# Kernel optimization log

Measured on AMD Instinct MI355X. Metric: run time of the kernel, lower is better.

## Reference

```python
import jax, jax.numpy as jnp
import numpy as np

N, F_IN, D_MID, D_HID, H, G, D_TGT = 6144, 128, 128, 64, 4, 12, 16
LEAKY_ALPHA = 0.2
EPS = 1e-9


def setup_inputs() -> dict:
    key = jax.random.key(0)
    ks = jax.random.split(key, 12)
    x = jax.random.normal(ks[0], (N, F_IN), dtype=jnp.float32)
    # 12 graphs of 512 nodes each (sorted segment ids)
    batch = jnp.repeat(jnp.arange(G, dtype=jnp.int32), N // G)
    # counting_attn is block-diagonal per graph with nonnegative random walk counts
    block = (batch[:, None] == batch[None, :]).astype(jnp.float32)
    counting_attn = jax.random.uniform(ks[1], (N, N), dtype=jnp.float32) * block
    s = lambda d: 1.0 / np.sqrt(d).astype(np.float32)
    Wv = jax.random.normal(ks[2], (F_IN, D_MID), jnp.float32) * s(F_IN)
    bv = jnp.zeros((D_MID,), jnp.float32)
    W0 = jax.random.normal(ks[3], (H, D_MID, D_HID), jnp.float32) * s(D_MID)
    al0 = jax.random.normal(ks[4], (H, D_HID), jnp.float32) * s(D_HID)
    ar0 = jax.random.normal(ks[5], (H, D_HID), jnp.float32) * s(D_HID)
    Wf = jax.random.normal(ks[6], (H * D_HID, D_MID), jnp.float32) * s(H * D_HID)
    alf = jax.random.normal(ks[7], (D_MID,), jnp.float32) * s(D_MID)
    arf = jax.random.normal(ks[8], (D_MID,), jnp.float32) * s(D_MID)
    W1 = jax.random.normal(ks[9], (D_MID, D_MID), jnp.float32) * s(D_MID)
    b1 = jnp.zeros((D_MID,), jnp.float32)
    W2 = jax.random.normal(ks[10], (D_MID, D_TGT), jnp.float32) * s(D_MID)
    b2 = jnp.zeros((D_TGT,), jnp.float32)
    return dict(x=x, counting_attn=counting_attn, batch=batch,
                Wv=Wv, bv=bv, W0=W0, al0=al0, ar0=ar0,
                Wf=Wf, alf=alf, arf=arf, W1=W1, b1=b1, W2=W2, b2=b2)


def gwk_head(h, mask, W, al, ar):
    # GWKLayer: elementwise score, LeakyReLU, masked softmax (via max-sub + exp*mask), weighted sum, ELU
    ft = h @ W  # [N, D]
    a1 = jnp.einsum('nd,d->n', ft, al)  # [N]
    a2 = jnp.einsum('nd,d->n', ft, ar)  # [N]
    a = jax.nn.leaky_relu(a1[:, None] + a2[None, :], LEAKY_ALPHA)  # [N, N]
    a = a - jnp.max(a, axis=1, keepdims=True)
    nomi = jnp.exp(a) * mask
    attn = nomi / (jnp.sum(nomi, axis=1, keepdims=True) + EPS)
    return jax.nn.elu(attn @ ft)  # [N, D]


def reference(x, counting_attn, batch, Wv, bv, W0, al0, ar0, Wf, alf, arf, W1, b1, W2, b2):
    # normalize == 'ones' -> no-op; dropout p = 0.0 (eval)
    h = jax.nn.relu(x @ Wv + bv)  # fc_before_gat: [N, D_MID]
    # layer 0: H parallel heads, concatenated along feature dim
    heads = jax.vmap(lambda W, al, ar: gwk_head(h, counting_attn, W, al, ar))(W0, al0, ar0)  # [H, N, D_HID]
    h = jnp.transpose(heads, (1, 0, 2)).reshape(N, H * D_HID)  # [N, 256]
    # final single-head layer back to D_MID
    h = gwk_head(h, counting_attn, Wf, alf, arf)  # [N, D_MID]
    # pooling 'mean' dispatches to global_add_pool (sum per graph) in the source
    pooled = jax.ops.segment_sum(h, batch, num_segments=G)  # [G, D_MID]
    out = jax.nn.relu(pooled @ W1 + b1) @ W2 + b2  # [G, D_TGT]
    return out
```

## Files before the change

### kernel.cpp

```cpp
#include <hip/hip_runtime.h>
#include <math.h>

#define Nn 6144
#define FIN 128
#define DMID 128
#define DHID 64
#define NH 4
#define NG 12
#define NB 512
#define ALPHA 0.2f
#define EPSV 1e-9f

typedef __bf16 bf16x8 __attribute__((ext_vector_type(8)));
typedef float f32x4 __attribute__((ext_vector_type(4)));
typedef unsigned short ushort_t;

union BU { bf16x8 v; uint u[4]; uint4 q; };

__device__ __forceinline__ float leaky(float x){ return x > 0.f ? x : ALPHA*x; }
__device__ __forceinline__ float eluf(float x){ return x > 0.f ? x : __expf(x)-1.f; }
__device__ __forceinline__ uint f2bf(float f){
  uint u = __float_as_uint(f);
  return (u + 0x7FFFu + ((u>>16)&1u)) >> 16;
}
__device__ __forceinline__ float wave_max(float v){
  #pragma unroll
  for (int off=32; off; off>>=1) v = fmaxf(v, __shfl_xor(v, off));
  return v;
}

__global__ __launch_bounds__(256) void k_prep(
    const float* __restrict__ Wv, const float* __restrict__ W0, const float* __restrict__ Wf,
    ushort_t* __restrict__ WvS, ushort_t* __restrict__ W0S, ushort_t* __restrict__ WfS){
  int tid = blockIdx.x*256 + threadIdx.x;
  int lane = tid & 63, blk = tid >> 6;
  if (blk >= 160) return;
  const float* src; ushort_t* dst; int N; size_t off;
  if (blk < 32){
    int nt = blk>>2, kt = blk&3;
    src = Wv; dst = WvS; N = 128;
    off = ((size_t)(nt*4+kt)*64 + lane)*8;
    int col = nt*16 + (lane&15); int k0 = kt*32 + (lane>>4)*8;
    uint4 pk;
    uint e0=f2bf(src[(k0+0)*N+col]), e1=f2bf(src[(k0+1)*N+col]);
    uint e2=f2bf(src[(k0+2)*N+col]), e3=f2bf(src[(k0+3)*N+col]);
    uint e4=f2bf(src[(k0+4)*N+col]), e5=f2bf(src[(k0+5)*N+col]);
    uint e6=f2bf(src[(k0+6)*N+col]), e7=f2bf(src[(k0+7)*N+col]);
    pk.x=e0|(e1<<16); pk.y=e2|(e3<<16); pk.z=e4|(e5<<16); pk.w=e6|(e7<<16);
    *reinterpret_cast<uint4*>(dst + off) = pk;
  } else if (blk < 96){
    int b2 = blk-32; int hd = b2>>4, r = b2&15; int nt = r>>2, kt = r&3;
    src = W0 + (size_t)hd*128*64; dst = W0S + (size_t)hd*8192; N = 64;
    off = ((size_t)(nt*4+kt)*64 + lane)*8;
    int col = nt*16 + (lane&15); int k0 = kt*32 + (lane>>4)*8;
    uint4 pk;
    uint e0=f2bf(src[(k0+0)*N+col]), e1=f2bf(src[(k0+1)*N+col]);
    uint e2=f2bf(src[(k0+2)*N+col]), e3=f2bf(src[(k0+3)*N+col]);
    uint e4=f2bf(src[(k0+4)*N+col]), e5=f2bf(src[(k0+5)*N+col]);
    uint e6=f2bf(src[(k0+6)*N+col]), e7=f2bf(src[(k0+7)*N+col]);
    pk.x=e0|(e1<<16); pk.y=e2|(e3<<16); pk.z=e4|(e5<<16); pk.w=e6|(e7<<16);
    *reinterpret_cast<uint4*>(dst + off) = pk;
  } else {
    int b2 = blk-96; int nt = b2>>3, kt = b2&7;
    src = Wf; dst = WfS; N = 128;
    off = ((size_t)(nt*8+kt)*64 + lane)*8;
    int col = nt*16 + (lane&15); int k0 = kt*32 + (lane>>4)*8;
    uint4 pk;
    uint e0=f2bf(src[(k0+0)*N+col]), e1=f2bf(src[(k0+1)*N+col]);
    uint e2=f2bf(src[(k0+2)*N+col]), e3=f2bf(src[(k0+3)*N+col]);
    uint e4=f2bf(src[(k0+4)*N+col]), e5=f2bf(src[(k0+5)*N+col]);
    uint e6=f2bf(src[(k0+6)*N+col]), e7=f2bf(src[(k0+7)*N+col]);
    pk.x=e0|(e1<<16); pk.y=e2|(e3<<16); pk.z=e4|(e5<<16); pk.w=e6|(e7<<16);
    *reinterpret_cast<uint4*>(dst + off) = pk;
  }
}

__global__ __launch_bounds__(256) void k_f1(
    const float* __restrict__ x, const float* __restrict__ bv,
    const ushort_t* __restrict__ WvS, const ushort_t* __restrict__ W0S,
    const float* __restrict__ al0, const float* __restrict__ ar0,
    ushort_t* __restrict__ ftS, float* __restrict__ a1arr, float* __restrict__ a2arr,
    float* __restrict__ pmax0){
  int b = blockIdx.x; int i0 = b*16;
  int t = threadIdx.x, lane = t&63, w = t>>6;
  int row = lane&15, kg = lane>>4;
  __shared__ ushort_t xs[16][136];
  __shared__ ushort_t hts[16][136];
  __shared__ ushort_t fts[16][264];
  {
    const float* xp = x + (size_t)i0*FIN + t*8;
    float4 f0 = *reinterpret_cast<const float4*>(xp);
    float4 f1 = *reinterpret_cast<const float4*>(xp+4);
    uint4 pk;
    pk.x = f2bf(f0.x)|(f2bf(f0.y)<<16); pk.y = f2bf(f0.z)|(f2bf(f0.w)<<16);
    pk.z = f2bf(f1.x)|(f2bf(f1.y)<<16); pk.w = f2bf(f1.z)|(f2bf(f1.w)<<16);
    *reinterpret_cast<uint4*>(&xs[t>>4][(t&15)*8]) = pk;
  }
  __syncthreads();
  {
    f32x4 acc2[2] = {{0,0,0,0},{0,0,0,0}};
    #pragma unroll
    for (int kt=0; kt<4; ++kt){
      bf16x8 aF = *reinterpret_cast<bf16x8*>(&xs[row][kt*32 + kg*8]);
      #pragma unroll
      for (int e2=0; e2<2; ++e2){
        int nt = w*2+e2;
        BU B; B.q = *reinterpret_cast<const uint4*>(WvS + ((size_t)(nt*4+kt)*64 + lane)*8);
        acc2[e2] = __builtin_amdgcn_mfma_f32_16x16x32_bf16(aF, B.v, acc2[e2], 0, 0, 0);
      }
    }
    #pragma unroll
    for (int e2=0; e2<2; ++e2){
      int nt = w*2+e2;
      float bvv = bv[nt*16+row];
      #pragma unroll
      for (int reg=0; reg<4; ++reg){
        float v = fmaxf(acc2[e2][reg]+bvv, 0.f);
        hts[kg*4+reg][nt*16+row] = (ushort_t)f2bf(v);
      }
    }
  }
  __syncthreads();
  f32x4 acc4[4] = {{0,0,0,0},{0,0,0,0},{0,0,0,0},{0,0,0,0}};
  #pragma unroll
  for (int kt=0; kt<4; ++kt){
    bf16x8 aF = *reinterpret_cast<bf16x8*>(&hts[row][kt*32 + kg*8]);
    #pragma unroll
    for (int nt=0; nt<4; ++nt){
      BU B; B.q = *reinterpret_cast<const uint4*>(W0S + ((size_t)((w*4+nt)*4+kt)*64 + lane)*8);
      acc4[nt] = __builtin_amdgcn_mfma_f32_16x16x32_bf16(aF, B.v, acc4[nt], 0, 0, 0);
    }
  }
  {
    float alv[4], arv[4];
    #pragma unroll
    for (int nt=0; nt<4; ++nt){ alv[nt] = al0[w*DHID+nt*16+row]; arv[nt] = ar0[w*DHID+nt*16+row]; }
    float s1[4]={0,0,0,0}, s2[4]={0,0,0,0};
    #pragma unroll
    for (int nt=0; nt<4; ++nt)
      #pragma unroll
      for (int reg=0; reg<4; ++reg){
        s1[reg] += acc4[nt][reg]*alv[nt];
        s2[reg] += acc4[nt][reg]*arv[nt];
      }
    #pragma unroll
    for (int off=1; off<16; off<<=1)
      #pragma unroll
      for (int reg=0; reg<4; ++reg){
        s1[reg] += __shfl_xor(s1[reg], off);
        s2[reg] += __shfl_xor(s2[reg], off);
      }
    if (row==0){
      #pragma unroll
      for (int reg=0; reg<4; ++reg){
        a1arr[w*Nn + i0 + kg*4+reg] = s1[reg];
        a2arr[w*Nn + i0 + kg*4+reg] = s2[reg];
      }
    }
    float mm = fmaxf(fmaxf(s2[0],s2[1]), fmaxf(s2[2],s2[3]));
    mm = fmaxf(mm, __shfl_xor(mm,16));
    mm = fmaxf(mm, __shfl_xor(mm,32));
    if (lane==0) pmax0[w*384 + b] = mm;
  }
  #pragma unroll
  for (int nt=0; nt<4; ++nt)
    #pragma unroll
    for (int reg=0; reg<4; ++reg)
      fts[kg*4+reg][w*DHID + nt*16+row] = (ushort_t)f2bf(acc4[nt][reg]);
  __syncthreads();
  {
    int ch = t, hd2 = ch>>6, ct = (ch>>4)&3, c = ch&15;
    int g = b>>5, ktj = (b&31)>>1, half = b&1;
    ushort_t v[16];
    #pragma unroll
    for (int i=0; i<16; ++i) v[i] = fts[i][ch];
    uint4 p0, p1;
    p0.x=(uint)v[0]|((uint)v[1]<<16);  p0.y=(uint)v[2]|((uint)v[3]<<16);
    p0.z=(uint)v[4]|((uint)v[5]<<16);  p0.w=(uint)v[6]|((uint)v[7]<<16);
    p1.x=(uint)v[8]|((uint)v[9]<<16);  p1.y=(uint)v[10]|((uint)v[11]<<16);
    p1.z=(uint)v[12]|((uint)v[13]<<16);p1.w=(uint)v[14]|((uint)v[15]<<16);
    size_t base = (((size_t)(g*4+hd2)*16 + ktj)*4 + ct)*512;
    *reinterpret_cast<uint4*>(ftS + base + ((half*2+0)*16+c)*8) = p0;
    *reinterpret_cast<uint4*>(ftS + base + ((half*2+1)*16+c)*8) = p1;
  }
}

__global__ __launch_bounds__(512) void k_attn0fcf(
    const ushort_t* __restrict__ ftS, const float* __restrict__ a1arr,
    const float* __restrict__ a2arr, const float* __restrict__ pmax0,
    const float* __restrict__ mask, const ushort_t* __restrict__ WfS,
    const float* __restrict__ alf, const float* __restrict__ arf,
    ushort_t* __restrict__ ftfS, float* __restrict__ a1f, float* __restrict__ a2f,
    float* __restrict__ pmaxf){
  int b = blockIdx.x;
  int g = b>>5, it = b&31;
  int i0 = g*NB + it*16, jbase = g*NB;
  int t = threadIdx.x, lane = t&63, w = t>>6;
  int hd = w>>1, jh = w&1;
  int row = lane&15, kg = lane>>4;

  __shared__ float aacc[8][4][64][4];
  __shared__ float ad[8][16];
  __shared__ ushort_t h1s[16][264];
  __shared__ ushort_t fts[16][136];
  __shared__ float dpA[8][16], dpB[8][16];

  {
    float mxv = -INFINITY;
    #pragma unroll
    for (int q=0; q<6; ++q) mxv = fmaxf(mxv, pmax0[hd*384 + q*64 + lane]);
    mxv = wave_max(mxv);
    float a1v = a1arr[hd*Nn + i0 + row];
    float mv = leaky(a1v + mxv);
    f32x4 acc[4] = {{0,0,0,0},{0,0,0,0},{0,0,0,0},{0,0,0,0}};
    float dsum = 0.f;
    const float* mrow = mask + (size_t)(i0+row)*Nn;
    size_t fbase = ((size_t)(g*4+hd)*16*4)*512;
    #pragma unroll 2
    for (int c8=0; c8<8; ++c8){
      int kt = jh*8 + c8;
      int jc = jbase + kt*32 + kg*8;
      float4 mk0 = *reinterpret_cast<const float4*>(mrow + jc);
      float4 mk1 = *reinterpret_cast<const float4*>(mrow + jc + 4);
      float4 a20 = *reinterpret_cast<const float4*>(a2arr + hd*Nn + jc);
      float4 a21 = *reinterpret_cast<const float4*>(a2arr + hd*Nn + jc + 4);
      float a2l[8] = {a20.x,a20.y,a20.z,a20.w,a21.x,a21.y,a21.z,a21.w};
      float mkl[8] = {mk0.x,mk0.y,mk0.z,mk0.w,mk1.x,mk1.y,mk1.z,mk1.w};
      float wv[8];
      #pragma unroll
      for (int e=0;e<8;++e){
        float p = __expf(leaky(a1v + a2l[e]) - mv) * mkl[e];
        wv[e] = p; dsum += p;
      }
      BU A;
      #pragma unroll
      for (int q=0;q<4;++q) A.u[q] = f2bf(wv[2*q]) | (f2bf(wv[2*q+1])<<16);
      #pragma unroll
      for (int ct=0; ct<4; ++ct){
        BU B; B.q = *reinterpret_cast<const uint4*>(ftS + fbase + (size_t)(kt*4+ct)*512 + lane*8);
        acc[ct] = __builtin_amdgcn_mfma_f32_16x16x32_bf16(A.v, B.v, acc[ct], 0, 0, 0);
      }
    }
    dsum += __shfl_xor(dsum, 16);
    dsum += __shfl_xor(dsum, 32);
    if (lane < 16) ad[w][lane] = dsum;
    #pragma unroll
    for (int ct=0; ct<4; ++ct)
      *reinterpret_cast<float4*>(&aacc[w][ct][lane][0]) = (float4){acc[ct][0],acc[ct][1],acc[ct][2],acc[ct][3]};
  }
  __syncthreads();
  {
    int w0 = hd*2, w1 = hd*2+1;
    float dr[4];
    #pragma unroll
    for (int reg=0; reg<4; ++reg) dr[reg] = ad[w0][kg*4+reg] + ad[w1][kg*4+reg] + EPSV;
    #pragma unroll
    for (int ci=0; ci<2; ++ci){
      int ct = jh*2+ci;
      float4 A0 = *reinterpret_cast<float4*>(&aacc[w0][ct][lane][0]);
      float4 A1 = *reinterpret_cast<float4*>(&aacc[w1][ct][lane][0]);
      float tot[4] = {A0.x+A1.x, A0.y+A1.y, A0.z+A1.z, A0.w+A1.w};
      #pragma unroll
      for (int reg=0; reg<4; ++reg){
        float o = eluf(tot[reg]/dr[reg]);
        h1s[kg*4+reg][hd*64 + ct*16 + row] = (ushort_t)f2bf(o);
      }
    }
  }
  __syncthreads();
  {
    f32x4 acc2 = {0,0,0,0};
    #pragma unroll
    for (int kt=0; kt<8; ++kt){
      bf16x8 aF = *reinterpret_cast<bf16x8*>(&h1s[row][kt*32 + kg*8]);
      BU B; B.q = *reinterpret_cast<const uint4*>(WfS + ((size_t)(w*8+kt)*64 + lane)*8);
      acc2 = __builtin_amdgcn_mfma_f32_16x16x32_bf16(aF, B.v, acc2, 0, 0, 0);
    }
    float alv = alf[w*16+row], arv = arf[w*16+row];
    float s1[4], s2[4];
    #pragma unroll
    for (int reg=0; reg<4; ++reg){
      s1[reg] = acc2[reg]*alv;
      s2[reg] = acc2[reg]*arv;
      fts[kg*4+reg][w*16+row] = (ushort_t)f2bf(acc2[reg]);
    }
    #pragma unroll
    for (int off=1; off<16; off<<=1)
      #pragma unroll
      for (int reg=0; reg<4; ++reg){
        s1[reg] += __shfl_xor(s1[reg], off);
        s2[reg] += __shfl_xor(s2[reg], off);
      }
    if (row==0){
      #pragma unroll
      for (int reg=0; reg<4; ++reg){ dpA[w][kg*4+reg]=s1[reg]; dpB[w][kg*4+reg]=s2[reg]; }
    }
  }
  __syncthreads();
  if (t < 16){
    float v1=0.f, v2=0.f;
    #pragma unroll
    for (int q=0; q<8; ++q){ v1 += dpA[q][t]; v2 += dpB[q][t]; }
    a1f[i0+t] = v1; a2f[i0+t] = v2;
    float m = v2;
    #pragma unroll
    for (int off=1; off<16; off<<=1) m = fmaxf(m, __shfl_xor(m, off));
    if (t==0) pmaxf[b] = m;
  }
  if (t < 256){
    int ch = t>>1, half8 = t&1;
    int ct = ch>>4, c = ch&15;
    int gg = b>>5, ktj = (b&31)>>1, half = b&1;
    ushort_t v[8];
    #pragma unroll
    for (int i=0; i<8; ++i) v[i] = fts[half8*8+i][ch];
    uint4 pk;
    pk.x=(uint)v[0]|((uint)v[1]<<16); pk.y=(uint)v[2]|((uint)v[3]<<16);
    pk.z=(uint)v[4]|((uint)v[5]<<16); pk.w=(uint)v[6]|((uint)v[7]<<16);
    int kslot = half*2 + half8;
    size_t base = ((size_t)(gg*16+ktj)*8 + ct)*512;
    *reinterpret_cast<uint4*>(ftfS + base + (kslot*16+c)*8) = pk;
  }
}

__global__ __launch_bounds__(256) void k_attnf(
    const ushort_t* __restrict__ ftfS, const float* __restrict__ a1f,
    const float* __restrict__ a2f, const float* __restrict__ pmaxf,
    const float* __restrict__ mask, float* __restrict__ ppart){
  int b = blockIdx.x;
  int g = b>>5, it = b&31;
  int i0 = g*NB + it*16, jbase = g*NB;
  int t = threadIdx.x, lane = t&63, w = t>>6;
  int row = lane&15, kg = lane>>4;
  __shared__ float s_acc[4][8][64][4];
  __shared__ float s_d[4][16];
  float mxv = -INFINITY;
  #pragma unroll
  for (int q=0; q<6; ++q) mxv = fmaxf(mxv, pmaxf[q*64 + lane]);
  mxv = wave_max(mxv);
  float a1v = a1f[i0+row];
  float mv = leaky(a1v + mxv);
  f32x4 acc[8];
  #pragma unroll
  for (int ct=0; ct<8; ++ct) acc[ct] = (f32x4){0,0,0,0};
  float dsum = 0.f;
  const float* mrow = mask + (size_t)(i0+row)*Nn;
  #pragma unroll 2
  for (int c4=0; c4<4; ++c4){
    int kt = w*4 + c4;
    int jc = jbase + kt*32 + kg*8;
    float4 mk0 = *reinterpret_cast<const float4*>(mrow + jc);
    float4 mk1 = *reinterpret_cast<const float4*>(mrow + jc + 4);
    float4 a20 = *reinterpret_cast<const float4*>(a2f + jc);
    float4 a21 = *reinterpret_cast<const float4*>(a2f + jc + 4);
    float a2l[8] = {a20.x,a20.y,a20.z,a20.w,a21.x,a21.y,a21.z,a21.w};
    float mkl[8] = {mk0.x,mk0.y,mk0.z,mk0.w,mk1.x,mk1.y,mk1.z,mk1.w};
    float wv[8];
    #pragma unroll
    for (int e=0;e<8;++e){
      float p = __expf(leaky(a1v + a2l[e]) - mv) * mkl[e];
      wv[e] = p; dsum += p;
    }
    BU A;
    #pragma unroll
    for (int q=0;q<4;++q) A.u[q] = f2bf(wv[2*q]) | (f2bf(wv[2*q+1])<<16);
    #pragma unroll
    for (int ct=0; ct<8; ++ct){
      BU B; B.q = *reinterpret_cast<const uint4*>(ftfS + ((size_t)(g*16+kt)*8 + ct)*512 + lane*8);
      acc[ct] = __builtin_amdgcn_mfma_f32_16x16x32_bf16(A.v, B.v, acc[ct], 0, 0, 0);
    }
  }
  dsum += __shfl_xor(dsum, 16);
  dsum += __shfl_xor(dsum, 32);
  if (lane < 16) s_d[w][lane] = dsum;
  #pragma unroll
  for (int ct=0; ct<8; ++ct)
    *reinterpret_cast<float4*>(&s_acc[w][ct][lane][0]) = (float4){acc[ct][0],acc[ct][1],acc[ct][2],acc[ct][3]};
  __syncthreads();
  float dr[4];
  #pragma unroll
  for (int reg=0; reg<4; ++reg)
    dr[reg] = s_d[0][kg*4+reg] + s_d[1][kg*4+reg] + s_d[2][kg*4+reg] + s_d[3][kg*4+reg] + EPSV;
  #pragma unroll
  for (int ci=0; ci<2; ++ci){
    int ct = w*2 + ci;
    float4 A0 = *reinterpret_cast<float4*>(&s_acc[0][ct][lane][0]);
    float4 A1 = *reinterpret_cast<float4*>(&s_acc[1][ct][lane][0]);
    float4 A2 = *reinterpret_cast<float4*>(&s_acc[2][ct][lane][0]);
    float4 A3 = *reinterpret_cast<float4*>(&s_acc[3][ct][lane][0]);
    float tot[4] = {A0.x+A1.x+A2.x+A3.x, A0.y+A1.y+A2.y+A3.y,
                    A0.z+A1.z+A2.z+A3.z, A0.w+A1.w+A2.w+A3.w};
    float psum = 0.f;
    #pragma unroll
    for (int reg=0; reg<4; ++reg) psum += eluf(tot[reg]/dr[reg]);
    psum += __shfl_xor(psum, 16);
    psum += __shfl_xor(psum, 32);
    if (lane < 16) ppart[(size_t)b*DMID + ct*16 + lane] = psum;
  }
}

__global__ __launch_bounds__(256) void k_mlp(
    const float* __restrict__ ppart, const float* __restrict__ W1, const float* __restrict__ b1,
    const float* __restrict__ W2, const float* __restrict__ b2, float* __restrict__ out){
  int g = blockIdx.x;
  int t = threadIdx.x;
  __shared__ float red[8][DMID];
  __shared__ float ps[DMID], ts[DMID];
  __shared__ float p2[2][DMID];
  __shared__ float p4[2][16];
  {
    float4 s4 = {0,0,0,0};
    #pragma unroll
    for (int gi=0; gi<4; ++gi){
      int itx = (t>>5) + gi*8;
      float4 v = *reinterpret_cast<const float4*>(ppart + (size_t)(g*32+itx)*DMID + (t&31)*4);
      s4.x += v.x; s4.y += v.y; s4.z += v.z; s4.w += v.w;
    }
    *reinterpret_cast<float4*>(&red[t>>5][(t&31)*4]) = s4;
  }
  __syncthreads();
  if (t < DMID){
    float s = 0.f;
    #pragma unroll
    for (int q=0; q<8; ++q) s += red[q][t];
    ps[t] = s;
  }
  __syncthreads();
  {
    int col = t & 127, half = t>>7;
    float acc = 0.f;
    #pragma unroll 8
    for (int k=half*64; k<half*64+64; ++k) acc += ps[k]*W1[k*DMID+col];
    p2[half][col] = acc;
  }
  __syncthreads();
  if (t < DMID) ts[t] = fmaxf(p2[0][t]+p2[1][t]+b1[t], 0.f);
  __syncthreads();
  if (t < 32){
    int col = t & 15, half = t>>4;
    float acc = 0.f;
    #pragma unroll 8
    for (int k=half*64; k<half*64+64; ++k) acc += ts[k]*W2[k*16+col];
    p4[half][col] = acc;
  }
  __syncthreads();
  if (t < 16) out[g*16+t] = p4[0][t]+p4[1][t]+b2[t];
}

extern "C" void kernel_launch(void* const* d_in, const int* in_sizes, int n_in,
                              void* d_out, int out_size, void* d_ws, size_t ws_size,
                              hipStream_t stream) {
  const float* x    = (const float*)d_in[0];
  const float* mask = (const float*)d_in[1];
  const float* Wv   = (const float*)d_in[3];
  const float* bv   = (const float*)d_in[4];
  const float* W0   = (const float*)d_in[5];
  const float* al0  = (const float*)d_in[6];
  const float* ar0  = (const float*)d_in[7];
  const float* Wf   = (const float*)d_in[8];
  const float* alf  = (const float*)d_in[9];
  const float* arf  = (const float*)d_in[10];
  const float* W1   = (const float*)d_in[11];
  const float* b1   = (const float*)d_in[12];
  const float* W2   = (const float*)d_in[13];
  const float* b2   = (const float*)d_in[14];
  float* out = (float*)d_out;

  char* W = (char*)d_ws;
  ushort_t* WvS  = (ushort_t*)(W);
  ushort_t* W0S  = (ushort_t*)(W + 32768);
  ushort_t* WfS  = (ushort_t*)(W + 98304);
  ushort_t* ftS  = (ushort_t*)(W + 163840);
  ushort_t* ftfS = (ushort_t*)(W + 3309568);
  float* a1arr = (float*)(W + 4882432);
  float* a2arr = (float*)(W + 4980736);
  float* a1f   = (float*)(W + 5079040);
  float* a2f   = (float*)(W + 5103616);
  float* pmax0 = (float*)(W + 5128192);
  float* pmaxf = (float*)(W + 5134336);
  float* ppart = (float*)(W + 5135872);

  hipLaunchKernelGGL(k_prep,     dim3(40),    dim3(256), 0, stream, Wv, W0, Wf, WvS, W0S, WfS);
  hipLaunchKernelGGL(k_f1,       dim3(Nn/16), dim3(256), 0, stream,
                     x, bv, WvS, W0S, al0, ar0, ftS, a1arr, a2arr, pmax0);
  hipLaunchKernelGGL(k_attn0fcf, dim3(NG*32), dim3(512), 0, stream,
                     ftS, a1arr, a2arr, pmax0, mask, WfS, alf, arf, ftfS, a1f, a2f, pmaxf);
  hipLaunchKernelGGL(k_attnf,    dim3(NG*32), dim3(256), 0, stream,
                     ftfS, a1f, a2f, pmaxf, mask, ppart);
  hipLaunchKernelGGL(k_mlp,      dim3(NG),    dim3(256), 0, stream,
                     ppart, W1, b1, W2, b2, out);
}
```

Baseline: 57.50 us.

## Fuse weight prep into f1 and MLP into final attention via tickets

Removes the separate weight-packing kernel by having each f1 block pack Wv/W0 into shared memory (and 8 blocks pack Wf to global). It also folds the MLP into the last attention kernel, using a per-graph atomic ticket so the last-finishing block does the pooling and MLP. Block count is halved to 192 with 512 threads handling 32 rows each, and the split-j reduction in attn0 is replaced by full-K loops per wave. The aim is fewer launches and less smem reduction traffic. The cost is redundant weight packing in every f1 block and lower grid parallelism.

```diff
diff --git a/kernel.cpp b/kernel.cpp
--- a/kernel.cpp
+++ b/kernel.cpp
@@ -28,113 +28,103 @@
   for (int off=32; off; off>>=1) v = fmaxf(v, __shfl_xor(v, off));
   return v;
 }
-
-__global__ __launch_bounds__(256) void k_prep(
-    const float* __restrict__ Wv, const float* __restrict__ W0, const float* __restrict__ Wf,
-    ushort_t* __restrict__ WvS, ushort_t* __restrict__ W0S, ushort_t* __restrict__ WfS){
-  int tid = blockIdx.x*256 + threadIdx.x;
-  int lane = tid & 63, blk = tid >> 6;
-  if (blk >= 160) return;
-  const float* src; ushort_t* dst; int N; size_t off;
-  if (blk < 32){
-    int nt = blk>>2, kt = blk&3;
-    src = Wv; dst = WvS; N = 128;
-    off = ((size_t)(nt*4+kt)*64 + lane)*8;
-    int col = nt*16 + (lane&15); int k0 = kt*32 + (lane>>4)*8;
-    uint4 pk;
-    uint e0=f2bf(src[(k0+0)*N+col]), e1=f2bf(src[(k0+1)*N+col]);
-    uint e2=f2bf(src[(k0+2)*N+col]), e3=f2bf(src[(k0+3)*N+col]);
-    uint e4=f2bf(src[(k0+4)*N+col]), e5=f2bf(src[(k0+5)*N+col]);
-    uint e6=f2bf(src[(k0+6)*N+col]), e7=f2bf(src[(k0+7)*N+col]);
-    pk.x=e0|(e1<<16); pk.y=e2|(e3<<16); pk.z=e4|(e5<<16); pk.w=e6|(e7<<16);
-    *reinterpret_cast<uint4*>(dst + off) = pk;
-  } else if (blk < 96){
-    int b2 = blk-32; int hd = b2>>4, r = b2&15; int nt = r>>2, kt = r&3;
-    src = W0 + (size_t)hd*128*64; dst = W0S + (size_t)hd*8192; N = 64;
-    off = ((size_t)(nt*4+kt)*64 + lane)*8;
-    int col = nt*16 + (lane&15); int k0 = kt*32 + (lane>>4)*8;
-    uint4 pk;
-    uint e0=f2bf(src[(k0+0)*N+col]), e1=f2bf(src[(k0+1)*N+col]);
-    uint e2=f2bf(src[(k0+2)*N+col]), e3=f2bf(src[(k0+3)*N+col]);
-    uint e4=f2bf(src[(k0+4)*N+col]), e5=f2bf(src[(k0+5)*N+col]);
-    uint e6=f2bf(src[(k0+6)*N+col]), e7=f2bf(src[(k0+7)*N+col]);
-    pk.x=e0|(e1<<16); pk.y=e2|(e3<<16); pk.z=e4|(e5<<16); pk.w=e6|(e7<<16);
-    *reinterpret_cast<uint4*>(dst + off) = pk;
-  } else {
-    int b2 = blk-96; int nt = b2>>3, kt = b2&7;
-    src = Wf; dst = WfS; N = 128;
-    off = ((size_t)(nt*8+kt)*64 + lane)*8;
-    int col = nt*16 + (lane&15); int k0 = kt*32 + (lane>>4)*8;
-    uint4 pk;
-    uint e0=f2bf(src[(k0+0)*N+col]), e1=f2bf(src[(k0+1)*N+col]);
-    uint e2=f2bf(src[(k0+2)*N+col]), e3=f2bf(src[(k0+3)*N+col]);
-    uint e4=f2bf(src[(k0+4)*N+col]), e5=f2bf(src[(k0+5)*N+col]);
-    uint e6=f2bf(src[(k0+6)*N+col]), e7=f2bf(src[(k0+7)*N+col]);
-    pk.x=e0|(e1<<16); pk.y=e2|(e3<<16); pk.z=e4|(e5<<16); pk.w=e6|(e7<<16);
-    *reinterpret_cast<uint4*>(dst + off) = pk;
-  }
-}
-
-__global__ __launch_bounds__(256) void k_f1(
-    const float* __restrict__ x, const float* __restrict__ bv,
-    const ushort_t* __restrict__ WvS, const ushort_t* __restrict__ W0S,
-    const float* __restrict__ al0, const float* __restrict__ ar0,
+__device__ __forceinline__ uint4 packW(const float* p, int strd){
+  uint4 pk;
+  pk.x = f2bf(p[0])      | (f2bf(p[strd])<<16);
+  pk.y = f2bf(p[2*strd]) | (f2bf(p[3*strd])<<16);
+  pk.z = f2bf(p[4*strd]) | (f2bf(p[5*strd])<<16);
+  pk.w = f2bf(p[6*strd]) | (f2bf(p[7*strd])<<16);
+  return pk;
+}
+
+__global__ __launch_bounds__(512) void k_f1(
+    const float* __restrict__ x, const float* __restrict__ Wv, const float* __restrict__ bv,
+    const float* __restrict__ W0, const float* __restrict__ al0, const float* __restrict__ ar0,
+    const float* __restrict__ Wf, ushort_t* __restrict__ WfS,
     ushort_t* __restrict__ ftS, float* __restrict__ a1arr, float* __restrict__ a2arr,
-    float* __restrict__ pmax0){
-  int b = blockIdx.x; int i0 = b*16;
-  int t = threadIdx.x, lane = t&63, w = t>>6;
+    float* __restrict__ pmax0, int* __restrict__ ticket){
+  int b = blockIdx.x, t = threadIdx.x;
+  int lane = t&63, w = t>>6;
   int row = lane&15, kg = lane>>4;
-  __shared__ ushort_t xs[16][136];
-  __shared__ ushort_t hts[16][136];
-  __shared__ ushort_t fts[16][264];
-  {
-    const float* xp = x + (size_t)i0*FIN + t*8;
+  int g = b>>4;
+
+  __shared__ ushort_t wvs[32*64*8];
+  __shared__ ushort_t w0s[64*64*8];
+  __shared__ ushort_t xs[2][16][136];
+  __shared__ ushort_t hts[2][16][136];
+  __shared__ ushort_t fts[2][16][264];
+
+  if (b == 0 && t < NG) ticket[t] = 0;
+  if (b < 8){
+    int s = b*512 + t;
+    int fb = s>>6, ln = s&63;
+    int nt = fb>>3, kt = fb&7;
+    int col = nt*16 + (ln&15), k0 = kt*32 + (ln>>4)*8;
+    *reinterpret_cast<uint4*>(WfS + (size_t)s*8) = packW(Wf + (size_t)k0*DMID + col, DMID);
+  }
+  for (int s = t; s < 2048; s += 512){
+    int fb = s>>6, ln = s&63;
+    int nt = fb>>2, kt = fb&3;
+    int col = nt*16 + (ln&15), k0 = kt*32 + (ln>>4)*8;
+    *reinterpret_cast<uint4*>(&wvs[(size_t)s*8]) = packW(Wv + (size_t)k0*DMID + col, DMID);
+  }
+  for (int s = t; s < 4096; s += 512){
+    int fb = s>>6, ln = s&63;
+    int hd = fb>>4, r = fb&15, nt = r>>2, kt = r&3;
+    int col = nt*16 + (ln&15), k0 = kt*32 + (ln>>4)*8;
+    *reinterpret_cast<uint4*>(&w0s[(size_t)s*8]) =
+        packW(W0 + (size_t)hd*DMID*DHID + (size_t)k0*DHID + col, DHID);
+  }
+  {
+    int n = t>>4;
+    const float* xp = x + (size_t)(b*32+n)*FIN + (t&15)*8;
     float4 f0 = *reinterpret_cast<const float4*>(xp);
     float4 f1 = *reinterpret_cast<const float4*>(xp+4);
     uint4 pk;
     pk.x = f2bf(f0.x)|(f2bf(f0.y)<<16); pk.y = f2bf(f0.z)|(f2bf(f0.w)<<16);
     pk.z = f2bf(f1.x)|(f2bf(f1.y)<<16); pk.w = f2bf(f1.z)|(f2bf(f1.w)<<16);
-    *reinterpret_cast<uint4*>(&xs[t>>4][(t&15)*8]) = pk;
-  }
-  __syncthreads();
-  {
+    *reinterpret_cast<uint4*>(&xs[n>>4][n&15][(t&15)*8]) = pk;
+  }
+  __syncthreads();
+  {
+    int ii = w>>2, p = w&3;
     f32x4 acc2[2] = {{0,0,0,0},{0,0,0,0}};
     #pragma unroll
     for (int kt=0; kt<4; ++kt){
-      bf16x8 aF = *reinterpret_cast<bf16x8*>(&xs[row][kt*32 + kg*8]);
+      bf16x8 aF = *reinterpret_cast<bf16x8*>(&xs[ii][row][kt*32 + kg*8]);
       #pragma unroll
       for (int e2=0; e2<2; ++e2){
-        int nt = w*2+e2;
-        BU B; B.q = *reinterpret_cast<const uint4*>(WvS + ((size_t)(nt*4+kt)*64 + lane)*8);
+        int nt = p*2+e2;
+        BU B; B.q = *reinterpret_cast<uint4*>(&wvs[((size_t)(nt*4+kt)*64 + lane)*8]);
         acc2[e2] = __builtin_amdgcn_mfma_f32_16x16x32_bf16(aF, B.v, acc2[e2], 0, 0, 0);
       }
     }
     #pragma unroll
     for (int e2=0; e2<2; ++e2){
-      int nt = w*2+e2;
+      int nt = p*2+e2;
       float bvv = bv[nt*16+row];
       #pragma unroll
-      for (int reg=0; reg<4; ++reg){
-        float v = fmaxf(acc2[e2][reg]+bvv, 0.f);
-        hts[kg*4+reg][nt*16+row] = (ushort_t)f2bf(v);
-      }
-    }
-  }
-  __syncthreads();
-  f32x4 acc4[4] = {{0,0,0,0},{0,0,0,0},{0,0,0,0},{0,0,0,0}};
-  #pragma unroll
-  for (int kt=0; kt<4; ++kt){
-    bf16x8 aF = *reinterpret_cast<bf16x8*>(&hts[row][kt*32 + kg*8]);
-    #pragma unroll
-    for (int nt=0; nt<4; ++nt){
-      BU B; B.q = *reinterpret_cast<const uint4*>(W0S + ((size_t)((w*4+nt)*4+kt)*64 + lane)*8);
-      acc4[nt] = __builtin_amdgcn_mfma_f32_16x16x32_bf16(aF, B.v, acc4[nt], 0, 0, 0);
-    }
-  }
-  {
+      for (int reg=0; reg<4; ++reg)
+        hts[ii][kg*4+reg][nt*16+row] = (ushort_t)f2bf(fmaxf(acc2[e2][reg]+bvv, 0.f));
+    }
+  }
+  __syncthreads();
+  {
+    int ii = w>>2, hd = w&3;
+    int i0 = b*32 + ii*16;
+    f32x4 acc4[4] = {{0,0,0,0},{0,0,0,0},{0,0,0,0},{0,0,0,0}};
+    #pragma unroll
+    for (int kt=0; kt<4; ++kt){
+      bf16x8 aF = *reinterpret_cast<bf16x8*>(&hts[ii][row][kt*32 + kg*8]);
+      #pragma unroll
+      for (int nt=0; nt<4; ++nt){
+        BU B; B.q = *reinterpret_cast<uint4*>(&w0s[(((size_t)(hd*4+nt)*4+kt)*64 + lane)*8]);
+        acc4[nt] = __builtin_amdgcn_mfma_f32_16x16x32_bf16(aF, B.v, acc4[nt], 0, 0, 0);
+      }
+    }
     float alv[4], arv[4];
     #pragma unroll
-    for (int nt=0; nt<4; ++nt){ alv[nt] = al0[w*DHID+nt*16+row]; arv[nt] = ar0[w*DHID+nt*16+row]; }
+    for (int nt=0; nt<4; ++nt){ alv[nt] = al0[hd*DHID+nt*16+row]; arv[nt] = ar0[hd*DHID+nt*16+row]; }
     float s1[4]={0,0,0,0}, s2[4]={0,0,0,0};
     #pragma unroll
     for (int nt=0; nt<4; ++nt)
@@ -153,27 +143,28 @@
     if (row==0){
       #pragma unroll
       for (int reg=0; reg<4; ++reg){
-        a1arr[w*Nn + i0 + kg*4+reg] = s1[reg];
-        a2arr[w*Nn + i0 + kg*4+reg] = s2[reg];
+        a1arr[hd*Nn + i0 + kg*4+reg] = s1[reg];
+        a2arr[hd*Nn + i0 + kg*4+reg] = s2[reg];
       }
     }
     float mm = fmaxf(fmaxf(s2[0],s2[1]), fmaxf(s2[2],s2[3]));
     mm = fmaxf(mm, __shfl_xor(mm,16));
     mm = fmaxf(mm, __shfl_xor(mm,32));
-    if (lane==0) pmax0[w*384 + b] = mm;
-  }
-  #pragma unroll
-  for (int nt=0; nt<4; ++nt)
-    #pragma unroll
-    for (int reg=0; reg<4; ++reg)
-      fts[kg*4+reg][w*DHID + nt*16+row] = (ushort_t)f2bf(acc4[nt][reg]);
-  __syncthreads();
-  {
-    int ch = t, hd2 = ch>>6, ct = (ch>>4)&3, c = ch&15;
-    int g = b>>5, ktj = (b&31)>>1, half = b&1;
+    if (lane==0) pmax0[hd*384 + b*2 + ii] = mm;
+    #pragma unroll
+    for (int nt=0; nt<4; ++nt)
+      #pragma unroll
+      for (int reg=0; reg<4; ++reg)
+        fts[ii][kg*4+reg][hd*DHID + nt*16+row] = (ushort_t)f2bf(acc4[nt][reg]);
+  }
+  __syncthreads();
+  {
+    int iw = t>>8, tt = t&255;
+    int hd2 = tt>>6, ct = (tt>>4)&3, c = tt&15;
+    int ktj = b&15, half = iw;
     ushort_t v[16];
     #pragma unroll
-    for (int i=0; i<16; ++i) v[i] = fts[i][ch];
+    for (int i=0; i<16; ++i) v[i] = fts[iw][i][tt];
     uint4 p0, p1;
     p0.x=(uint)v[0]|((uint)v[1]<<16);  p0.y=(uint)v[2]|((uint)v[3]<<16);
     p0.z=(uint)v[4]|((uint)v[5]<<16);  p0.w=(uint)v[6]|((uint)v[7]<<16);
@@ -192,18 +183,17 @@
     const float* __restrict__ alf, const float* __restrict__ arf,
     ushort_t* __restrict__ ftfS, float* __restrict__ a1f, float* __restrict__ a2f,
     float* __restrict__ pmaxf){
-  int b = blockIdx.x;
-  int g = b>>5, it = b&31;
-  int i0 = g*NB + it*16, jbase = g*NB;
-  int t = threadIdx.x, lane = t&63, w = t>>6;
-  int hd = w>>1, jh = w&1;
+  int b = blockIdx.x, t = threadIdx.x;
+  int lane = t&63, w = t>>6;
   int row = lane&15, kg = lane>>4;
-
-  __shared__ float aacc[8][4][64][4];
-  __shared__ float ad[8][16];
-  __shared__ ushort_t h1s[16][264];
-  __shared__ ushort_t fts[16][136];
-  __shared__ float dpA[8][16], dpB[8][16];
+  int g = b>>4;
+  int ii = w>>2, hd = w&3;
+  int i0 = b*32 + ii*16;
+  int jbase = g*NB;
+
+  __shared__ ushort_t h1s[2][16][264];
+  __shared__ ushort_t fts[2][16][136];
+  __shared__ float dpA[2][4][16], dpB[2][4][16];
 
   {
     float mxv = -INFINITY;
@@ -215,10 +205,9 @@
     f32x4 acc[4] = {{0,0,0,0},{0,0,0,0},{0,0,0,0},{0,0,0,0}};
     float dsum = 0.f;
     const float* mrow = mask + (size_t)(i0+row)*Nn;
-    size_t fbase = ((size_t)(g*4+hd)*16*4)*512;
+    size_t fbase = ((size_t)(g*4+hd)*64)*512;
     #pragma unroll 2
-    for (int c8=0; c8<8; ++c8){
-      int kt = jh*8 + c8;
+    for (int kt=0; kt<16; ++kt){
       int jc = jbase + kt*32 + kg*8;
       float4 mk0 = *reinterpret_cast<const float4*>(mrow + jc);
       float4 mk1 = *reinterpret_cast<const float4*>(mrow + jc + 4);
@@ -237,52 +226,47 @@
       for (int q=0;q<4;++q) A.u[q] = f2bf(wv[2*q]) | (f2bf(wv[2*q+1])<<16);
       #pragma unroll
       for (int ct=0; ct<4; ++ct){
-        BU B; B.q = *reinterpret_cast<const uint4*>(ftS + fbase + (size_t)(kt*4+ct)*512 + lane*8);
+        BU B;
+        B.q = *reinterpret_cast<const uint4*>(ftS + fbase + (size_t)(kt*4+ct)*512 + lane*8);
         acc[ct] = __builtin_amdgcn_mfma_f32_16x16x32_bf16(A.v, B.v, acc[ct], 0, 0, 0);
       }
     }
     dsum += __shfl_xor(dsum, 16);
     dsum += __shfl_xor(dsum, 32);
-    if (lane < 16) ad[w][lane] = dsum;
     #pragma unroll
     for (int ct=0; ct<4; ++ct)
-      *reinterpret_cast<float4*>(&aacc[w][ct][lane][0]) = (float4){acc[ct][0],acc[ct][1],acc[ct][2],acc[ct][3]};
-  }
-  __syncthreads();
-  {
-    int w0 = hd*2, w1 = hd*2+1;
-    float dr[4];
-    #pragma unroll
-    for (int reg=0; reg<4; ++reg) dr[reg] = ad[w0][kg*4+reg] + ad[w1][kg*4+reg] + EPSV;
-    #pragma unroll
-    for (int ci=0; ci<2; ++ci){
-      int ct = jh*2+ci;
-      float4 A0 = *reinterpret_cast<float4*>(&aacc[w0][ct][lane][0]);
-      float4 A1 = *reinterpret_cast<float4*>(&aacc[w1][ct][lane][0]);
-      float tot[4] = {A0.x+A1.x, A0.y+A1.y, A0.z+A1.z, A0.w+A1.w};
-      #pragma unroll
-      for (int reg=0; reg<4; ++reg){
-        float o = eluf(tot[reg]/dr[reg]);
-        h1s[kg*4+reg][hd*64 + ct*16 + row] = (ushort_t)f2bf(o);
-      }
-    }
-  }
-  __syncthreads();
-  {
-    f32x4 acc2 = {0,0,0,0};
+      #pragma unroll
+      for (int reg=0; reg<4; ++reg){
+        float drow = __shfl(dsum, kg*4+reg) + EPSV;
+        float o = eluf(acc[ct][reg] / drow);
+        h1s[ii][kg*4+reg][hd*DHID + ct*16 + row] = (ushort_t)f2bf(o);
+      }
+  }
+  __syncthreads();
+  {
+    int p = w&3;
+    f32x4 acc2[2] = {{0,0,0,0},{0,0,0,0}};
     #pragma unroll
     for (int kt=0; kt<8; ++kt){
-      bf16x8 aF = *reinterpret_cast<bf16x8*>(&h1s[row][kt*32 + kg*8]);
-      BU B; B.q = *reinterpret_cast<const uint4*>(WfS + ((size_t)(w*8+kt)*64 + lane)*8);
-      acc2 = __builtin_amdgcn_mfma_f32_16x16x32_bf16(aF, B.v, acc2, 0, 0, 0);
-    }
-    float alv = alf[w*16+row], arv = arf[w*16+row];
-    float s1[4], s2[4];
-    #pragma unroll
-    for (int reg=0; reg<4; ++reg){
-      s1[reg] = acc2[reg]*alv;
-      s2[reg] = acc2[reg]*arv;
-      fts[kg*4+reg][w*16+row] = (ushort_t)f2bf(acc2[reg]);
+      bf16x8 aF = *reinterpret_cast<bf16x8*>(&h1s[ii][row][kt*32 + kg*8]);
+      #pragma unroll
+      for (int e2=0; e2<2; ++e2){
+        int nt = p*2+e2;
+        BU B; B.q = *reinterpret_cast<const uint4*>(WfS + ((size_t)(nt*8+kt)*64 + lane)*8);
+        acc2[e2] = __builtin_amdgcn_mfma_f32_16x16x32_bf16(aF, B.v, acc2[e2], 0, 0, 0);
+      }
+    }
+    float s1[4]={0,0,0,0}, s2[4]={0,0,0,0};
+    #pragma unroll
+    for (int e2=0; e2<2; ++e2){
+      int nt = p*2+e2;
+      float alv = alf[nt*16+row], arv = arf[nt*16+row];
+      #pragma unroll
+      for (int reg=0; reg<4; ++reg){
+        s1[reg] += acc2[e2][reg]*alv;
+        s2[reg] += acc2[e2][reg]*arv;
+        fts[ii][kg*4+reg][nt*16+row] = (ushort_t)f2bf(acc2[e2][reg]);
+      }
     }
     #pragma unroll
     for (int off=1; off<16; off<<=1)
@@ -293,158 +277,169 @@
       }
     if (row==0){
       #pragma unroll
-      for (int reg=0; reg<4; ++reg){ dpA[w][kg*4+reg]=s1[reg]; dpB[w][kg*4+reg]=s2[reg]; }
-    }
-  }
-  __syncthreads();
-  if (t < 16){
-    float v1=0.f, v2=0.f;
-    #pragma unroll
-    for (int q=0; q<8; ++q){ v1 += dpA[q][t]; v2 += dpB[q][t]; }
-    a1f[i0+t] = v1; a2f[i0+t] = v2;
+      for (int reg=0; reg<4; ++reg){ dpA[ii][p][kg*4+reg]=s1[reg]; dpB[ii][p][kg*4+reg]=s2[reg]; }
+    }
+  }
+  __syncthreads();
+  if (t < 32){
+    int iw = t>>4, r = t&15;
+    float v1 = dpA[iw][0][r]+dpA[iw][1][r]+dpA[iw][2][r]+dpA[iw][3][r];
+    float v2 = dpB[iw][0][r]+dpB[iw][1][r]+dpB[iw][2][r]+dpB[iw][3][r];
+    int node = b*32 + iw*16 + r;
+    a1f[node] = v1; a2f[node] = v2;
     float m = v2;
     #pragma unroll
-    for (int off=1; off<16; off<<=1) m = fmaxf(m, __shfl_xor(m, off));
+    for (int off=1; off<32; off<<=1) m = fmaxf(m, __shfl_xor(m, off));
     if (t==0) pmaxf[b] = m;
   }
-  if (t < 256){
-    int ch = t>>1, half8 = t&1;
+  {
+    int iw = t>>8, tt = t&255;
+    int ch = tt>>1, half8 = tt&1;
     int ct = ch>>4, c = ch&15;
-    int gg = b>>5, ktj = (b&31)>>1, half = b&1;
+    int ktj = b&15;
     ushort_t v[8];
     #pragma unroll
-    for (int i=0; i<8; ++i) v[i] = fts[half8*8+i][ch];
+    for (int i=0; i<8; ++i) v[i] = fts[iw][half8*8+i][ch];
     uint4 pk;
     pk.x=(uint)v[0]|((uint)v[1]<<16); pk.y=(uint)v[2]|((uint)v[3]<<16);
     pk.z=(uint)v[4]|((uint)v[5]<<16); pk.w=(uint)v[6]|((uint)v[7]<<16);
-    int kslot = half*2 + half8;
-    size_t base = ((size_t)(gg*16+ktj)*8 + ct)*512;
+    int kslot = iw*2 + half8;
+    size_t base = ((size_t)(g*16+ktj)*8 + ct)*512;
     *reinterpret_cast<uint4*>(ftfS + base + (kslot*16+c)*8) = pk;
   }
 }
 
-__global__ __launch_bounds__(256) void k_attnf(
+__global__ __launch_bounds__(512) void k_attnfmlp(
     const ushort_t* __restrict__ ftfS, const float* __restrict__ a1f,
     const float* __restrict__ a2f, const float* __restrict__ pmaxf,
-    const float* __restrict__ mask, float* __restrict__ ppart){
-  int b = blockIdx.x;
-  int g = b>>5, it = b&31;
-  int i0 = g*NB + it*16, jbase = g*NB;
-  int t = threadIdx.x, lane = t&63, w = t>>6;
+    const float* __restrict__ mask,
+    const float* __restrict__ W1, const float* __restrict__ b1,
+    const float* __restrict__ W2, const float* __restrict__ b2,
+    float* __restrict__ ppart, int* __restrict__ ticket, float* __restrict__ out){
+  int b = blockIdx.x, t = threadIdx.x;
+  int lane = t&63, w = t>>6;
   int row = lane&15, kg = lane>>4;
-  __shared__ float s_acc[4][8][64][4];
-  __shared__ float s_d[4][16];
-  float mxv = -INFINITY;
-  #pragma unroll
-  for (int q=0; q<6; ++q) mxv = fmaxf(mxv, pmaxf[q*64 + lane]);
-  mxv = wave_max(mxv);
-  float a1v = a1f[i0+row];
-  float mv = leaky(a1v + mxv);
-  f32x4 acc[8];
-  #pragma unroll
-  for (int ct=0; ct<8; ++ct) acc[ct] = (f32x4){0,0,0,0};
-  float dsum = 0.f;
-  const float* mrow = mask + (size_t)(i0+row)*Nn;
-  #pragma unroll 2
-  for (int c4=0; c4<4; ++c4){
-    int kt = w*4 + c4;
-    int jc = jbase + kt*32 + kg*8;
-    float4 mk0 = *reinterpret_cast<const float4*>(mrow + jc);
-    float4 mk1 = *reinterpret_cast<const float4*>(mrow + jc + 4);
-    float4 a20 = *reinterpret_cast<const float4*>(a2f + jc);
-    float4 a21 = *reinterpret_cast<const float4*>(a2f + jc + 4);
-    float a2l[8] = {a20.x,a20.y,a20.z,a20.w,a21.x,a21.y,a21.z,a21.w};
-    float mkl[8] = {mk0.x,mk0.y,mk0.z,mk0.w,mk1.x,mk1.y,mk1.z,mk1.w};
-    float wv[8];
-    #pragma unroll
-    for (int e=0;e<8;++e){
-      float p = __expf(leaky(a1v + a2l[e]) - mv) * mkl[e];
-      wv[e] = p; dsum += p;
-    }
-    BU A;
-    #pragma unroll
-    for (int q=0;q<4;++q) A.u[q] = f2bf(wv[2*q]) | (f2bf(wv[2*q+1])<<16);
-    #pragma unroll
-    for (int ct=0; ct<8; ++ct){
-      BU B; B.q = *reinterpret_cast<const uint4*>(ftfS + ((size_t)(g*16+kt)*8 + ct)*512 + lane*8);
-      acc[ct] = __builtin_amdgcn_mfma_f32_16x16x32_bf16(A.v, B.v, acc[ct], 0, 0, 0);
-    }
-  }
-  dsum += __shfl_xor(dsum, 16);
-  dsum += __shfl_xor(dsum, 32);
-  if (lane < 16) s_d[w][lane] = dsum;
-  #pragma unroll
-  for (int ct=0; ct<8; ++ct)
-    *reinterpret_cast<float4*>(&s_acc[w][ct][lane][0]) = (float4){acc[ct][0],acc[ct][1],acc[ct][2],acc[ct][3]};
-  __syncthreads();
-  float dr[4];
-  #pragma unroll
-  for (int reg=0; reg<4; ++reg)
-    dr[reg] = s_d[0][kg*4+reg] + s_d[1][kg*4+reg] + s_d[2][kg*4+reg] + s_d[3][kg*4+reg] + EPSV;
-  #pragma unroll
-  for (int ci=0; ci<2; ++ci){
-    int ct = w*2 + ci;
-    float4 A0 = *reinterpret_cast<float4*>(&s_acc[0][ct][lane][0]);
-    float4 A1 = *reinterpret_cast<float4*>(&s_acc[1][ct][lane][0]);
-    float4 A2 = *reinterpret_cast<float4*>(&s_acc[2][ct][lane][0]);
-    float4 A3 = *reinterpret_cast<float4*>(&s_acc[3][ct][lane][0]);
-    float tot[4] = {A0.x+A1.x+A2.x+A3.x, A0.y+A1.y+A2.y+A3.y,
-                    A0.z+A1.z+A2.z+A3.z, A0.w+A1.w+A2.w+A3.w};
-    float psum = 0.f;
-    #pragma unroll
-    for (int reg=0; reg<4; ++reg) psum += eluf(tot[reg]/dr[reg]);
-    psum += __shfl_xor(psum, 16);
-    psum += __shfl_xor(psum, 32);
-    if (lane < 16) ppart[(size_t)b*DMID + ct*16 + lane] = psum;
-  }
-}
-
-__global__ __launch_bounds__(256) void k_mlp(
-    const float* __restrict__ ppart, const float* __restrict__ W1, const float* __restrict__ b1,
-    const float* __restrict__ W2, const float* __restrict__ b2, float* __restrict__ out){
-  int g = blockIdx.x;
-  int t = threadIdx.x;
-  __shared__ float red[8][DMID];
+  int g = b>>4;
+  int ii = w>>2, jq = w&3;
+  int i0 = b*32 + ii*16;
+  int jbase = g*NB;
+
+  __shared__ float s_acc[2][4][8][64][4];
+  __shared__ float s_d[2][4][16];
+  __shared__ float red[4][DMID];
   __shared__ float ps[DMID], ts[DMID];
-  __shared__ float p2[2][DMID];
   __shared__ float p4[2][16];
-  {
-    float4 s4 = {0,0,0,0};
-    #pragma unroll
-    for (int gi=0; gi<4; ++gi){
-      int itx = (t>>5) + gi*8;
-      float4 v = *reinterpret_cast<const float4*>(ppart + (size_t)(g*32+itx)*DMID + (t&31)*4);
-      s4.x += v.x; s4.y += v.y; s4.z += v.z; s4.w += v.w;
-    }
-    *reinterpret_cast<float4*>(&red[t>>5][(t&31)*4]) = s4;
-  }
-  __syncthreads();
-  if (t < DMID){
-    float s = 0.f;
-    #pragma unroll
-    for (int q=0; q<8; ++q) s += red[q][t];
-    ps[t] = s;
-  }
-  __syncthreads();
-  {
-    int col = t & 127, half = t>>7;
-    float acc = 0.f;
-    #pragma unroll 8
-    for (int k=half*64; k<half*64+64; ++k) acc += ps[k]*W1[k*DMID+col];
-    p2[half][col] = acc;
-  }
-  __syncthreads();
-  if (t < DMID) ts[t] = fmaxf(p2[0][t]+p2[1][t]+b1[t], 0.f);
-  __syncthreads();
-  if (t < 32){
-    int col = t & 15, half = t>>4;
-    float acc = 0.f;
-    #pragma unroll 8
-    for (int k=half*64; k<half*64+64; ++k) acc += ts[k]*W2[k*16+col];
-    p4[half][col] = acc;
-  }
-  __syncthreads();
-  if (t < 16) out[g*16+t] = p4[0][t]+p4[1][t]+b2[t];
+  __shared__ int flag;
+
+  {
+    float mxv = -INFINITY;
+    #pragma unroll
+    for (int q=0; q<3; ++q) mxv = fmaxf(mxv, pmaxf[q*64 + lane]);
+    mxv = wave_max(mxv);
+    float a1v = a1f[i0+row];
+    float mv = leaky(a1v + mxv);
+    f32x4 acc[8];
+    #pragma unroll
+    for (int ct=0; ct<8; ++ct) acc[ct] = (f32x4){0,0,0,0};
+    float dsum = 0.f;
+    const float* mrow = mask + (size_t)(i0+row)*Nn;
+    #pragma unroll 2
+    for (int c4=0; c4<4; ++c4){
+      int kt = jq*4 + c4;
+      int jc = jbase + kt*32 + kg*8;
+      float4 mk0 = *reinterpret_cast<const float4*>(mrow + jc);
+      float4 mk1 = *reinterpret_cast<const float4*>(mrow + jc + 4);
+      float4 a20 = *reinterpret_cast<const float4*>(a2f + jc);
+      float4 a21 = *reinterpret_cast<const float4*>(a2f + jc + 4);
+      float a2l[8] = {a20.x,a20.y,a20.z,a20.w,a21.x,a21.y,a21.z,a21.w};
+      float mkl[8] = {mk0.x,mk0.y,mk0.z,mk0.w,mk1.x,mk1.y,mk1.z,mk1.w};
+      float wv[8];
+      #pragma unroll
+      for (int e=0;e<8;++e){
+        float p = __expf(leaky(a1v + a2l[e]) - mv) * mkl[e];
+        wv[e] = p; dsum += p;
+      }
+      BU A;
+      #pragma unroll
+      for (int q=0;q<4;++q) A.u[q] = f2bf(wv[2*q]) | (f2bf(wv[2*q+1])<<16);
+      #pragma unroll
+      for (int ct=0; ct<8; ++ct){
+        BU B;
+        B.q = *reinterpret_cast<const uint4*>(ftfS + ((size_t)(g*16+kt)*8 + ct)*512 + lane*8);
+        acc[ct] = __builtin_amdgcn_mfma_f32_16x16x32_bf16(A.v, B.v, acc[ct], 0, 0, 0);
+      }
+    }
+    dsum += __shfl_xor(dsum, 16);
+    dsum += __shfl_xor(dsum, 32);
+    if (lane < 16) s_d[ii][jq][lane] = dsum;
+    #pragma unroll
+    for (int ct=0; ct<8; ++ct)
+      *reinterpret_cast<float4*>(&s_acc[ii][jq][ct][lane][0]) =
+          (float4){acc[ct][0],acc[ct][1],acc[ct][2],acc[ct][3]};
+  }
+  __syncthreads();
+  {
+    float dr[4];
+    #pragma unroll
+    for (int reg=0; reg<4; ++reg)
+      dr[reg] = s_d[ii][0][kg*4+reg] + s_d[ii][1][kg*4+reg]
+              + s_d[ii][2][kg*4+reg] + s_d[ii][3][kg*4+reg] + EPSV;
+    #pragma unroll
+    for (int ci=0; ci<2; ++ci){
+      int ct = jq*2 + ci;
+      float4 A0 = *reinterpret_cast<float4*>(&s_acc[ii][0][ct][lane][0]);
+      float4 A1 = *reinterpret_cast<float4*>(&s_acc[ii][1][ct][lane][0]);
+      float4 A2 = *reinterpret_cast<float4*>(&s_acc[ii][2][ct][lane][0]);
+      float4 A3 = *reinterpret_cast<float4*>(&s_acc[ii][3][ct][lane][0]);
+      float tot[4] = {A0.x+A1.x+A2.x+A3.x, A0.y+A1.y+A2.y+A3.y,
+                      A0.z+A1.z+A2.z+A3.z, A0.w+A1.w+A2.w+A3.w};
+      float psum = 0.f;
+      #pragma unroll
+      for (int reg=0; reg<4; ++reg) psum += eluf(tot[reg]/dr[reg]);
+      psum += __shfl_xor(psum, 16);
+      psum += __shfl_xor(psum, 32);
+      if (lane < 16) ppart[(size_t)(b*2+ii)*DMID + ct*16 + lane] = psum;
+    }
+  }
+  __threadfence();
+  __syncthreads();
+  if (t == 0){
+    int old = atomicAdd(&ticket[g], 1);
+    flag = (old == 15) ? 1 : 0;
+  }
+  __syncthreads();
+  if (flag){
+    __threadfence();
+    {
+      int part = t>>7, col = t&127;
+      float s = 0.f;
+      #pragma unroll
+      for (int q=0; q<8; ++q) s += ppart[(size_t)(g*32 + part*8 + q)*DMID + col];
+      red[part][col] = s;
+    }
+    __syncthreads();
+    if (t < DMID) ps[t] = red[0][t]+red[1][t]+red[2][t]+red[3][t];
+    __syncthreads();
+    if (t < 256){
+      int col = t&127, half = t>>7;
+      float accv = 0.f;
+      #pragma unroll 8
+      for (int k=half*64; k<half*64+64; ++k) accv += ps[k]*W1[k*DMID+col];
+      red[half][col] = accv;
+    }
+    __syncthreads();
+    if (t < DMID) ts[t] = fmaxf(red[0][t]+red[1][t]+b1[t], 0.f);
+    __syncthreads();
+    if (t < 32){
+      int col = t&15, half = t>>4;
+      float accv = 0.f;
+      #pragma unroll 8
+      for (int k=half*64; k<half*64+64; ++k) accv += ts[k]*W2[k*16+col];
+      p4[half][col] = accv;
+    }
+    __syncthreads();
+    if (t < 16) out[g*16+t] = p4[0][t]+p4[1][t]+b2[t];
+  }
 }
 
 extern "C" void kernel_launch(void* const* d_in, const int* in_sizes, int n_in,
@@ -467,26 +462,22 @@
   float* out = (float*)d_out;
 
   char* W = (char*)d_ws;
-  ushort_t* WvS  = (ushort_t*)(W);
-  ushort_t* W0S  = (ushort_t*)(W + 32768);
-  ushort_t* WfS  = (ushort_t*)(W + 98304);
-  ushort_t* ftS  = (ushort_t*)(W + 163840);
-  ushort_t* ftfS = (ushort_t*)(W + 3309568);
-  float* a1arr = (float*)(W + 4882432);
-  float* a2arr = (float*)(W + 4980736);
-  float* a1f   = (float*)(W + 5079040);
-  float* a2f   = (float*)(W + 5103616);
-  float* pmax0 = (float*)(W + 5128192);
-  float* pmaxf = (float*)(W + 5134336);
-  float* ppart = (float*)(W + 5135872);
-
-  hipLaunchKernelGGL(k_prep,     dim3(40),    dim3(256), 0, stream, Wv, W0, Wf, WvS, W0S, WfS);
-  hipLaunchKernelGGL(k_f1,       dim3(Nn/16), dim3(256), 0, stream,
-                     x, bv, WvS, W0S, al0, ar0, ftS, a1arr, a2arr, pmax0);
-  hipLaunchKernelGGL(k_attn0fcf, dim3(NG*32), dim3(512), 0, stream,
+  ushort_t* WfS  = (ushort_t*)(W);
+  ushort_t* ftS  = (ushort_t*)(W + 65536);
+  ushort_t* ftfS = (ushort_t*)(W + 3211264);
+  float* a1arr = (float*)(W + 4784128);
+  float* a2arr = (float*)(W + 4882432);
+  float* a1f   = (float*)(W + 4980736);
+  float* a2f   = (float*)(W + 5005312);
+  float* pmax0 = (float*)(W + 5029888);
+  float* pmaxf = (float*)(W + 5036032);
+  float* ppart = (float*)(W + 5036800);
+  int*   ticket= (int*)  (W + 5233408);
+
+  hipLaunchKernelGGL(k_f1,       dim3(192), dim3(512), 0, stream,
+                     x, Wv, bv, W0, al0, ar0, Wf, WfS, ftS, a1arr, a2arr, pmax0, ticket);
+  hipLaunchKernelGGL(k_attn0fcf, dim3(192), dim3(512), 0, stream,
                      ftS, a1arr, a2arr, pmax0, mask, WfS, alf, arf, ftfS, a1f, a2f, pmaxf);
-  hipLaunchKernelGGL(k_attnf,    dim3(NG*32), dim3(256), 0, stream,
-                     ftfS, a1f, a2f, pmaxf, mask, ppart);
-  hipLaunchKernelGGL(k_mlp,      dim3(NG),    dim3(256), 0, stream,
-                     ppart, W1, b1, W2, b2, out);
-}
+  hipLaunchKernelGGL(k_attnfmlp, dim3(192), dim3(512), 0, stream,
+                     ftfS, a1f, a2f, pmaxf, mask, W1, b1, W2, b2, ppart, ticket, out);
+}
```

Measured after the change: 89.42 us. +55.5%, slower.
